# Kernel optimization log

Measured on AMD Instinct MI355X. Metric: run time of the kernel, lower is better.

The kernel has to match this reference:

```python
import jax, jax.numpy as jnp
import numpy as np

N = 200000   # real nodes
P = 10       # num_parts (virtual nodes)
IN = 256     # in_channels
HID = 256    # hidden_channels
DCD = 256    # decode_channels (use_jk=False -> == hidden)
OUT = 64     # out_channels


def layer_norm(x, g, b, eps=1e-5):
    mu = jnp.mean(x, axis=-1, keepdims=True)
    var = jnp.var(x, axis=-1, keepdims=True)
    return (x - mu) * jax.lax.rsqrt(var + eps) * g + b


def setup_inputs() -> dict:
    key = jax.random.key(0)
    ks = jax.random.split(key, 16)
    s = lambda d: 1.0 / np.sqrt(d)
    return {
        "x": jax.random.normal(ks[0], (N + P, IN), dtype=jnp.float32),
        "mapping": jax.random.randint(ks[1], (N,), 0, P, dtype=jnp.int32),
        "vnode_embed": jax.random.normal(ks[2], (P, IN), dtype=jnp.float32),
        "vnode_bias_hid": 0.1 * jax.random.normal(ks[3], (P, HID), dtype=jnp.float32),
        "vnode_bias_dcd": 0.1 * jax.random.normal(ks[4], (P, DCD), dtype=jnp.float32),
        "W_in2hid": s(IN) * jax.random.normal(ks[5], (IN, HID), dtype=jnp.float32),
        "b_in2hid": jnp.zeros((HID,), dtype=jnp.float32),
        "g_ln_hid": jnp.ones((HID,), dtype=jnp.float32),
        "b_ln_hid": jnp.zeros((HID,), dtype=jnp.float32),
        "W_enc": s(HID) * jax.random.normal(ks[6], (HID, DCD), dtype=jnp.float32),
        "b_enc": jnp.zeros((DCD,), dtype=jnp.float32),
        "g_ln_enc": jnp.ones((DCD,), dtype=jnp.float32),
        "b_ln_enc": jnp.zeros((DCD,), dtype=jnp.float32),
        "W_aggr": s(2 * DCD) * jax.random.normal(ks[7], (2 * DCD, DCD), dtype=jnp.float32),
        "b_aggr": jnp.zeros((DCD,), dtype=jnp.float32),
        "W_out": s(DCD) * jax.random.normal(ks[8], (DCD, OUT), dtype=jnp.float32),
        "b_out": jnp.zeros((OUT,), dtype=jnp.float32),
    }


def reference(x, mapping, vnode_embed, vnode_bias_hid, vnode_bias_dcd,
              W_in2hid, b_in2hid, g_ln_hid, b_ln_hid,
              W_enc, b_enc, g_ln_enc, b_ln_enc,
              W_aggr, b_aggr, W_out, b_out):
    p = vnode_embed.shape[0]
    n = x.shape[0] - p
    # overwrite virtual-node rows with learned embeddings
    x = x.at[-p:].set(vnode_embed)
    # in2hid -> LayerNorm -> ELU
    x = jax.nn.elu(layer_norm(x @ W_in2hid + b_in2hid, g_ln_hid, b_ln_hid))
    x = x.at[-p:].add(vnode_bias_hid)
    # encoder stub: single linear hidden->decode with ELU (loss := 0)
    x = jax.nn.elu(x @ W_enc + b_enc)
    # decode-stage virtual-node bias
    x = x.at[-p:].add(vnode_bias_dcd)
    v_x = x[-p:]                      # [P, DCD]
    gathered = v_x[mapping]           # irregular gather of virtual rows, [N, DCD]
    n_x = jnp.concatenate([x[:n], gathered], axis=1)   # [N, 2*DCD]
    n_x = jax.nn.elu(layer_norm(n_x @ W_aggr + b_aggr, g_ln_enc, b_ln_enc))
    # dropout: eval mode -> identity
    full = jnp.concatenate([n_x, v_x], axis=0)
    y = full @ W_out + b_out
    out = y[:n]                       # [N, OUT]
    return out
```

## Files before the change

### kernel.cpp

```cpp
#include <hip/hip_runtime.h>
#include <hip/hip_bf16.h>
#include <math.h>

typedef unsigned short u16;
typedef __attribute__((ext_vector_type(8))) short bf16x8;
typedef __attribute__((ext_vector_type(4))) float f32x4;
typedef __attribute__((ext_vector_type(4))) int i32x4;

#define PV 10

__device__ __forceinline__ float bf2f(u16 u){
  union{unsigned int i; float f;} v; v.i = ((unsigned int)u)<<16; return v.f;
}
__device__ __forceinline__ u16 f2bf(float f){
  union{float f; unsigned int i;} v; v.f = f;
  unsigned int r = (v.i + 0x7FFFu + ((v.i>>16)&1u))>>16;
  return (u16)r;
}
__device__ __forceinline__ float eluf(float z){
  return z > 0.f ? z : (__expf(z) - 1.f);
}
__device__ __forceinline__ float ldp(const void* p, int i, int f32f){
  return f32f ? ((const float*)p)[i] : bf2f(((const u16*)p)[i]);
}
__device__ __forceinline__ int swz(int row, int cb){
  int m = ((row & 7) << 4) ^ ((row & 8) << 2);
  return (row << 9) + (cb ^ m);
}

__global__ void k_sniff(const u16* __restrict__ x, int* __restrict__ flag){
  int t = threadIdx.x;
  u16 u = x[2*t];
  int e = (u >> 7) & 0xFF;
  int sane = (e >= 113 && e <= 134) ? 1 : 0;
  unsigned long long b = __ballot(sane);
  if (t == 0) *flag = (__popcll(b) < 32) ? 1 : 0;
}

__global__ void k_fragpack(const int* __restrict__ flagp,
                           const void* __restrict__ W1, const void* __restrict__ W2,
                           const void* __restrict__ Wa, const void* __restrict__ Wo,
                           u16* __restrict__ W1F, u16* __restrict__ W2F,
                           u16* __restrict__ WaF, u16* __restrict__ WoF)
{
  const int f = *flagp;
  int idx = blockIdx.x * 256 + threadIdx.x;
  if (idx < 196608) {
    int local = idx & 65535;
    int which = idx >> 16;
    int j = local & 7;
    int fid = local >> 3;
    int lane = fid & 63, q = lane & 15, g = lane >> 4;
    int n = (fid >> 6) & 3;
    int s = (fid >> 8) & 7;
    int w = (fid >> 11) & 3;
    int col = 64*w + 16*n + q;
    int k = 32*s + 8*g + j;
    const void* src = which == 0 ? W1 : (which == 1 ? W2 : Wa);
    u16* dst = which == 0 ? W1F : (which == 1 ? W2F : WaF);
    dst[local] = f2bf(ldp(src, k*256 + col, f));
  } else if (idx < 212992) {
    int local = idx - 196608;
    int j = local & 7;
    int fid = local >> 3;
    int lane = fid & 63, q = lane & 15, g = lane >> 4;
    int n = (fid >> 6) & 3;
    int s = (fid >> 8) & 7;
    int col = 16*n + q;
    int k = 32*s + 8*g + j;
    WoF[local] = f2bf(ldp(Wo, k*64 + col, f));
  }
}

__global__ void k_vnode(const int* __restrict__ flagp,
                        const void* __restrict__ embed, const void* __restrict__ W1,
                        const void* __restrict__ b1, const void* __restrict__ g1, const void* __restrict__ bb1,
                        const void* __restrict__ vbh,
                        const void* __restrict__ W2, const void* __restrict__ b2,
                        const void* __restrict__ vbd,
                        const void* __restrict__ Wa, const void* __restrict__ ba,
                        float* __restrict__ vg)
{
  __shared__ float buf[PV][256];
  __shared__ float st[PV][2];
  const int f = *flagp;
  const int t = threadIdx.x;
  const int lane = t & 63;
  const int w = t >> 6;

  for (int r=0;r<PV;r++) buf[r][t] = ldp(embed, r*256 + t, f);
  __syncthreads();

  float acc[PV];

  #pragma unroll
  for (int r=0;r<PV;r++) acc[r] = 0.f;
  for (int k8=0;k8<32;k8++){
    float wf[8];
    #pragma unroll
    for (int j=0;j<8;j++) wf[j] = ldp(W1, (k8*8+j)*256 + t, f);
    #pragma unroll
    for (int r=0;r<PV;r++){
      f32x4 a0 = *(const f32x4*)(&buf[r][k8*8]);
      f32x4 a1 = *(const f32x4*)(&buf[r][k8*8+4]);
      acc[r] = fmaf(a0[0],wf[0],acc[r]); acc[r] = fmaf(a0[1],wf[1],acc[r]);
      acc[r] = fmaf(a0[2],wf[2],acc[r]); acc[r] = fmaf(a0[3],wf[3],acc[r]);
      acc[r] = fmaf(a1[0],wf[4],acc[r]); acc[r] = fmaf(a1[1],wf[5],acc[r]);
      acc[r] = fmaf(a1[2],wf[6],acc[r]); acc[r] = fmaf(a1[3],wf[7],acc[r]);
    }
  }
  {
    float bv = ldp(b1, t, f);
    #pragma unroll
    for (int r=0;r<PV;r++) acc[r] += bv;
  }
  __syncthreads();
  #pragma unroll
  for (int r=0;r<PV;r++) buf[r][t] = acc[r];
  __syncthreads();
  for (int r = w; r < PV; r += 4){
    float v0=buf[r][lane], v1=buf[r][lane+64], v2=buf[r][lane+128], v3=buf[r][lane+192];
    float s = v0+v1+v2+v3;
    float ss = v0*v0+v1*v1+v2*v2+v3*v3;
    #pragma unroll
    for (int off=1; off<64; off<<=1){ s += __shfl_xor(s,off,64); ss += __shfl_xor(ss,off,64); }
    if (lane==0){
      float mu = s*(1.f/256.f);
      float var = ss*(1.f/256.f) - mu*mu;
      st[r][0]=mu; st[r][1]=rsqrtf(var+1e-5f);
    }
  }
  __syncthreads();
  {
    float gv = ldp(g1,t,f), bbv = ldp(bb1,t,f);
    #pragma unroll
    for (int r=0;r<PV;r++){
      float v = (acc[r]-st[r][0])*st[r][1]*gv + bbv;
      buf[r][t] = eluf(v) + ldp(vbh, r*256+t, f);
    }
  }
  __syncthreads();

  #pragma unroll
  for (int r=0;r<PV;r++) acc[r] = 0.f;
  for (int k8=0;k8<32;k8++){
    float wf[8];
    #pragma unroll
    for (int j=0;j<8;j++) wf[j] = ldp(W2, (k8*8+j)*256 + t, f);
    #pragma unroll
    for (int r=0;r<PV;r++){
      f32x4 a0 = *(const f32x4*)(&buf[r][k8*8]);
      f32x4 a1 = *(const f32x4*)(&buf[r][k8*8+4]);
      acc[r] = fmaf(a0[0],wf[0],acc[r]); acc[r] = fmaf(a0[1],wf[1],acc[r]);
      acc[r] = fmaf(a0[2],wf[2],acc[r]); acc[r] = fmaf(a0[3],wf[3],acc[r]);
      acc[r] = fmaf(a1[0],wf[4],acc[r]); acc[r] = fmaf(a1[1],wf[5],acc[r]);
      acc[r] = fmaf(a1[2],wf[6],acc[r]); acc[r] = fmaf(a1[3],wf[7],acc[r]);
    }
  }
  __syncthreads();
  {
    float bv = ldp(b2,t,f);
    #pragma unroll
    for (int r=0;r<PV;r++) buf[r][t] = eluf(acc[r]+bv) + ldp(vbd, r*256+t, f);
  }
  __syncthreads();

  #pragma unroll
  for (int r=0;r<PV;r++) acc[r] = 0.f;
  for (int k8=0;k8<32;k8++){
    float wf[8];
    #pragma unroll
    for (int j=0;j<8;j++) wf[j] = ldp(Wa, (256 + k8*8+j)*256 + t, f);
    #pragma unroll
    for (int r=0;r<PV;r++){
      f32x4 a0 = *(const f32x4*)(&buf[r][k8*8]);
      f32x4 a1 = *(const f32x4*)(&buf[r][k8*8+4]);
      acc[r] = fmaf(a0[0],wf[0],acc[r]); acc[r] = fmaf(a0[1],wf[1],acc[r]);
      acc[r] = fmaf(a0[2],wf[2],acc[r]); acc[r] = fmaf(a0[3],wf[3],acc[r]);
      acc[r] = fmaf(a1[0],wf[4],acc[r]); acc[r] = fmaf(a1[1],wf[5],acc[r]);
      acc[r] = fmaf(a1[2],wf[6],acc[r]); acc[r] = fmaf(a1[3],wf[7],acc[r]);
    }
  }
  {
    float bv = ldp(ba,t,f);
    #pragma unroll
    for (int r=0;r<PV;r++) vg[r*256+t] = acc[r] + bv;
  }
}

__device__ __forceinline__ void ln_rows(f32x4 (&acc)[4][4], float2 (*part)[4], float2* stats,
                                        int tid, int wid, int q, int g)
{
  #pragma unroll
  for (int m=0;m<4;m++){
    #pragma unroll
    for (int j=0;j<4;j++){
      float s1=0.f, s2=0.f;
      #pragma unroll
      for (int n=0;n<4;n++){ float v = acc[m][n][j]; s1+=v; s2+=v*v; }
      s1 += __shfl_xor(s1,1,64); s2 += __shfl_xor(s2,1,64);
      s1 += __shfl_xor(s1,2,64); s2 += __shfl_xor(s2,2,64);
      s1 += __shfl_xor(s1,4,64); s2 += __shfl_xor(s2,4,64);
      s1 += __shfl_xor(s1,8,64); s2 += __shfl_xor(s2,8,64);
      if (q == 0) part[16*m + 4*g + j][wid] = make_float2(s1, s2);
    }
  }
  __syncthreads();
  if (tid < 64){
    float s=0.f, ss=0.f;
    #pragma unroll
    for (int w=0;w<4;w++){ float2 p = part[tid][w]; s+=p.x; ss+=p.y; }
    float mu = s*(1.f/256.f);
    float var = ss*(1.f/256.f) - mu*mu;
    stats[tid] = make_float2(mu, rsqrtf(var + 1e-5f));
  }
  __syncthreads();
}

__global__ __launch_bounds__(256, 2) void k_main(
    const int* __restrict__ flagp,
    const void* __restrict__ x, const int* __restrict__ mapping,
    const void* __restrict__ b1, const void* __restrict__ g1, const void* __restrict__ bb1,
    const void* __restrict__ b2,
    const void* __restrict__ g3, const void* __restrict__ bb3,
    const void* __restrict__ bo,
    const u16* __restrict__ W1F, const u16* __restrict__ W2F,
    const u16* __restrict__ WaF, const u16* __restrict__ WoF,
    const float* __restrict__ vg, void* __restrict__ out)
{
  __shared__ __align__(16) u16 Abuf[64*256];
  __shared__ float2 part[64][4];
  __shared__ float2 stats[64];
  __shared__ int maplds[64];

  const int f = *flagp;
  const int tid = threadIdx.x;
  const int wid = tid >> 6;
  const int lane = tid & 63;
  const int q = lane & 15;
  const int g = lane >> 4;
  const int R0 = blockIdx.x * 64;

  if (f) {
    const float* xr = (const float*)x + (size_t)R0 * 256;
    #pragma unroll
    for (int i=0;i<8;i++){
      int c = tid + 256*i;
      int row = c >> 5;
      int cb  = (c & 31) << 4;
      int e0  = (c & 31) << 3;
      float4 a = *(const float4*)(xr + row*256 + e0);
      float4 b = *(const float4*)(xr + row*256 + e0 + 4);
      union { u16 h[8]; i32x4 v; } pk;
      pk.h[0]=f2bf(a.x); pk.h[1]=f2bf(a.y); pk.h[2]=f2bf(a.z); pk.h[3]=f2bf(a.w);
      pk.h[4]=f2bf(b.x); pk.h[5]=f2bf(b.y); pk.h[6]=f2bf(b.z); pk.h[7]=f2bf(b.w);
      *(i32x4*)((char*)Abuf + swz(row, cb)) = pk.v;
    }
  } else {
    const u16* xr = (const u16*)x + (size_t)R0 * 256;
    #pragma unroll
    for (int i=0;i<8;i++){
      int c = tid + 256*i;
      int row = c >> 5;
      int cb  = (c & 31) << 4;
      i32x4 v = *(const i32x4*)(xr + row*256 + ((c&31)<<3));
      *(i32x4*)((char*)Abuf + swz(row, cb)) = v;
    }
  }
  if (tid < 64){
    int mv = mapping[R0 + tid];
    maplds[tid] = mv < 0 ? 0 : (mv > PV-1 ? PV-1 : mv);
  }
  __syncthreads();

  f32x4 acc[4][4];
  const int fbase = wid*16384 + lane*8;

  {
    #pragma unroll
    for (int n=0;n<4;n++){
      float bv = ldp(b1, 64*wid + 16*n + q, f);
      #pragma unroll
      for (int m=0;m<4;m++) acc[m][n] = (f32x4){bv,bv,bv,bv};
    }
    #pragma unroll
    for (int s=0;s<8;s++){
      bf16x8 af[4], bw[4];
      #pragma unroll
      for (int m=0;m<4;m++) af[m] = *(const bf16x8*)((const char*)Abuf + swz(16*m+q, 64*s+16*g));
      #pragma unroll
      for (int n=0;n<4;n++) bw[n] = *(const bf16x8*)(W1F + fbase + (s*4+n)*512);
      #pragma unroll
      for (int m=0;m<4;m++){
        #pragma unroll
        for (int n=0;n<4;n++)
          acc[m][n] = __builtin_amdgcn_mfma_f32_16x16x32_bf16(af[m], bw[n], acc[m][n], 0,0,0);
      }
    }
  }
  ln_rows(acc, part, stats, tid, wid, q, g);
  {
    float gam[4], bet[4];
    #pragma unroll
    for (int n=0;n<4;n++){ int col = 64*wid+16*n+q; gam[n]=ldp(g1,col,f); bet[n]=ldp(bb1,col,f); }
    #pragma unroll
    for (int m=0;m<4;m++){
      #pragma unroll
      for (int j=0;j<4;j++){
        int row = 16*m + 4*g + j;
        float2 st = stats[row];
        #pragma unroll
        for (int n=0;n<4;n++){
          float v = (acc[m][n][j] - st.x) * st.y * gam[n] + bet[n];
          *(u16*)((char*)Abuf + swz(row, (64*wid+16*n+q)<<1)) = f2bf(eluf(v));
        }
      }
    }
  }
  __syncthreads();

  {
    #pragma unroll
    for (int n=0;n<4;n++){
      float bv = ldp(b2, 64*wid + 16*n + q, f);
      #pragma unroll
      for (int m=0;m<4;m++) acc[m][n] = (f32x4){bv,bv,bv,bv};
    }
    #pragma unroll
    for (int s=0;s<8;s++){
      bf16x8 af[4], bw[4];
      #pragma unroll
      for (int m=0;m<4;m++) af[m] = *(const bf16x8*)((const char*)Abuf + swz(16*m+q, 64*s+16*g));
      #pragma unroll
      for (int n=0;n<4;n++) bw[n] = *(const bf16x8*)(W2F + fbase + (s*4+n)*512);
      #pragma unroll
      for (int m=0;m<4;m++){
        #pragma unroll
        for (int n=0;n<4;n++)
          acc[m][n] = __builtin_amdgcn_mfma_f32_16x16x32_bf16(af[m], bw[n], acc[m][n], 0,0,0);
      }
    }
  }
  __syncthreads();
  {
    #pragma unroll
    for (int m=0;m<4;m++){
      #pragma unroll
      for (int j=0;j<4;j++){
        int row = 16*m + 4*g + j;
        #pragma unroll
        for (int n=0;n<4;n++)
          *(u16*)((char*)Abuf + swz(row, (64*wid+16*n+q)<<1)) = f2bf(eluf(acc[m][n][j]));
      }
    }
  }
  __syncthreads();

  {
    #pragma unroll
    for (int m=0;m<4;m++){
      int mp[4];
      #pragma unroll
      for (int j=0;j<4;j++) mp[j] = maplds[16*m + 4*g + j];
      #pragma unroll
      for (int n=0;n<4;n++){
        int col = 64*wid + 16*n + q;
        #pragma unroll
        for (int j=0;j<4;j++) acc[m][n][j] = vg[mp[j]*256 + col];
      }
    }
    #pragma unroll
    for (int s=0;s<8;s++){
      bf16x8 af[4], bw[4];
      #pragma unroll
      for (int m=0;m<4;m++) af[m] = *(const bf16x8*)((const char*)Abuf + swz(16*m+q, 64*s+16*g));
      #pragma unroll
      for (int n=0;n<4;n++) bw[n] = *(const bf16x8*)(WaF + fbase + (s*4+n)*512);
      #pragma unroll
      for (int m=0;m<4;m++){
        #pragma unroll
        for (int n=0;n<4;n++)
          acc[m][n] = __builtin_amdgcn_mfma_f32_16x16x32_bf16(af[m], bw[n], acc[m][n], 0,0,0);
      }
    }
  }
  ln_rows(acc, part, stats, tid, wid, q, g);
  {
    float gam[4], bet[4];
    #pragma unroll
    for (int n=0;n<4;n++){ int col = 64*wid+16*n+q; gam[n]=ldp(g3,col,f); bet[n]=ldp(bb3,col,f); }
    #pragma unroll
    for (int m=0;m<4;m++){
      #pragma unroll
      for (int j=0;j<4;j++){
        int row = 16*m + 4*g + j;
        float2 st = stats[row];
        #pragma unroll
        for (int n=0;n<4;n++){
          float v = (acc[m][n][j] - st.x) * st.y * gam[n] + bet[n];
          *(u16*)((char*)Abuf + swz(row, (64*wid+16*n+q)<<1)) = f2bf(eluf(v));
        }
      }
    }
  }
  __syncthreads();

  {
    f32x4 a4[4];
    #pragma unroll
    for (int n=0;n<4;n++){ float bv = ldp(bo, 16*n+q, f); a4[n] = (f32x4){bv,bv,bv,bv}; }
    #pragma unroll
    for (int s=0;s<8;s++){
      bf16x8 af = *(const bf16x8*)((const char*)Abuf + swz(16*wid+q, 64*s+16*g));
      #pragma unroll
      for (int n=0;n<4;n++){
        bf16x8 bw = *(const bf16x8*)(WoF + (s*4+n)*512 + lane*8);
        a4[n] = __builtin_amdgcn_mfma_f32_16x16x32_bf16(af, bw, a4[n], 0,0,0);
      }
    }
    if (f){
      float* outf = (float*)out;
      #pragma unroll
      for (int n=0;n<4;n++){
        #pragma unroll
        for (int j=0;j<4;j++){
          int grow = R0 + 16*wid + 4*g + j;
          outf[(size_t)grow*64 + 16*n + q] = a4[n][j];
        }
      }
    } else {
      u16* outh = (u16*)out;
      #pragma unroll
      for (int n=0;n<4;n++){
        #pragma unroll
        for (int j=0;j<4;j++){
          int grow = R0 + 16*wid + 4*g + j;
          outh[(size_t)grow*64 + 16*n + q] = f2bf(a4[n][j]);
        }
      }
    }
  }
}

extern "C" void kernel_launch(void* const* d_in, const int* in_sizes, int n_in,
                              void* d_out, int out_size, void* d_ws, size_t ws_size,
                              hipStream_t stream)
{
  const void* x    = d_in[0];
  const int* mapping = (const int*)d_in[1];
  const void* embed= d_in[2];
  const void* vbh  = d_in[3];
  const void* vbd  = d_in[4];
  const void* W1   = d_in[5];
  const void* b1   = d_in[6];
  const void* g1   = d_in[7];
  const void* bb1  = d_in[8];
  const void* W2   = d_in[9];
  const void* b2   = d_in[10];
  const void* g3   = d_in[11];
  const void* bb3  = d_in[12];
  const void* Wa   = d_in[13];
  const void* ba   = d_in[14];
  const void* Wo   = d_in[15];
  const void* bo   = d_in[16];

  char* ws = (char*)d_ws;
  int* flagp = (int*)ws;
  u16* W1F = (u16*)(ws + 4096);
  u16* W2F = (u16*)(ws + 4096 + 131072);
  u16* WaF = (u16*)(ws + 4096 + 262144);
  u16* WoF = (u16*)(ws + 4096 + 393216);
  float* vg = (float*)(ws + 4096 + 425984);

  const int N = in_sizes[1];

  k_sniff<<<1, 64, 0, stream>>>((const u16*)x, flagp);
  k_fragpack<<<832, 256, 0, stream>>>(flagp, W1, W2, Wa, Wo, W1F, W2F, WaF, WoF);
  k_vnode<<<1, 256, 0, stream>>>(flagp, embed, W1, b1, g1, bb1, vbh, W2, b2, vbd, Wa, ba, vg);
  k_main<<<N/64, 256, 0, stream>>>(flagp, x, mapping, b1, g1, bb1, b2, g3, bb3, bo,
                                   W1F, W2F, WaF, WoF, vg, (void*)d_out);
}
```

Before: 309.1 us.

## Double rows per block to 128 and use packed bf16 conversion

```diff
diff --git a/kernel.cpp b/kernel.cpp
--- a/kernel.cpp
+++ b/kernel.cpp
@@ -3,6 +3,7 @@
 #include <math.h>
 
 typedef unsigned short u16;
+typedef unsigned int u32;
 typedef __attribute__((ext_vector_type(8))) short bf16x8;
 typedef __attribute__((ext_vector_type(4))) float f32x4;
 typedef __attribute__((ext_vector_type(4))) int i32x4;
@@ -16,6 +17,9 @@
   union{float f; unsigned int i;} v; v.f = f;
   unsigned int r = (v.i + 0x7FFFu + ((v.i>>16)&1u))>>16;
   return (u16)r;
+}
+__device__ __forceinline__ u32 cvtpk(float lo, float hi){
+  u32 r; asm("v_cvt_pk_bf16_f32 %0, %1, %2" : "=v"(r) : "v"(lo), "v"(hi)); return r;
 }
 __device__ __forceinline__ float eluf(float z){
   return z > 0.f ? z : (__expf(z) - 1.f);
@@ -188,37 +192,9 @@
   }
 }
 
-__device__ __forceinline__ void ln_rows(f32x4 (&acc)[4][4], float2 (*part)[4], float2* stats,
-                                        int tid, int wid, int q, int g)
-{
-  #pragma unroll
-  for (int m=0;m<4;m++){
-    #pragma unroll
-    for (int j=0;j<4;j++){
-      float s1=0.f, s2=0.f;
-      #pragma unroll
-      for (int n=0;n<4;n++){ float v = acc[m][n][j]; s1+=v; s2+=v*v; }
-      s1 += __shfl_xor(s1,1,64); s2 += __shfl_xor(s2,1,64);
-      s1 += __shfl_xor(s1,2,64); s2 += __shfl_xor(s2,2,64);
-      s1 += __shfl_xor(s1,4,64); s2 += __shfl_xor(s2,4,64);
-      s1 += __shfl_xor(s1,8,64); s2 += __shfl_xor(s2,8,64);
-      if (q == 0) part[16*m + 4*g + j][wid] = make_float2(s1, s2);
-    }
-  }
-  __syncthreads();
-  if (tid < 64){
-    float s=0.f, ss=0.f;
-    #pragma unroll
-    for (int w=0;w<4;w++){ float2 p = part[tid][w]; s+=p.x; ss+=p.y; }
-    float mu = s*(1.f/256.f);
-    float var = ss*(1.f/256.f) - mu*mu;
-    stats[tid] = make_float2(mu, rsqrtf(var + 1e-5f));
-  }
-  __syncthreads();
-}
-
+#define MROWS 128
 __global__ __launch_bounds__(256, 2) void k_main(
-    const int* __restrict__ flagp,
+    const int* __restrict__ flagp, int N,
     const void* __restrict__ x, const int* __restrict__ mapping,
     const void* __restrict__ b1, const void* __restrict__ g1, const void* __restrict__ bb1,
     const void* __restrict__ b2,
@@ -228,10 +204,11 @@
     const u16* __restrict__ WaF, const u16* __restrict__ WoF,
     const float* __restrict__ vg, void* __restrict__ out)
 {
-  __shared__ __align__(16) u16 Abuf[64*256];
-  __shared__ float2 part[64][4];
-  __shared__ float2 stats[64];
-  __shared__ int maplds[64];
+  extern __shared__ __align__(16) char smem[];
+  u16* Abuf = (u16*)smem;
+  float2 (*part)[4] = (float2(*)[4])(smem + 65536);
+  float2* stats = (float2*)(smem + 69632);
+  int* maplds = (int*)(smem + 70656);
 
   const int f = *flagp;
   const int tid = threadIdx.x;
@@ -239,41 +216,47 @@
   const int lane = tid & 63;
   const int q = lane & 15;
   const int g = lane >> 4;
-  const int R0 = blockIdx.x * 64;
+  const int R0 = blockIdx.x * MROWS;
 
   if (f) {
     const float* xr = (const float*)x + (size_t)R0 * 256;
     #pragma unroll
-    for (int i=0;i<8;i++){
+    for (int i=0;i<16;i++){
       int c = tid + 256*i;
       int row = c >> 5;
       int cb  = (c & 31) << 4;
       int e0  = (c & 31) << 3;
-      float4 a = *(const float4*)(xr + row*256 + e0);
-      float4 b = *(const float4*)(xr + row*256 + e0 + 4);
-      union { u16 h[8]; i32x4 v; } pk;
-      pk.h[0]=f2bf(a.x); pk.h[1]=f2bf(a.y); pk.h[2]=f2bf(a.z); pk.h[3]=f2bf(a.w);
-      pk.h[4]=f2bf(b.x); pk.h[5]=f2bf(b.y); pk.h[6]=f2bf(b.z); pk.h[7]=f2bf(b.w);
-      *(i32x4*)((char*)Abuf + swz(row, cb)) = pk.v;
+      i32x4 v;
+      if (R0 + row < N){
+        float4 a = *(const float4*)(xr + row*256 + e0);
+        float4 b = *(const float4*)(xr + row*256 + e0 + 4);
+        union { u32 u[4]; i32x4 v; } pk;
+        pk.u[0]=cvtpk(a.x,a.y); pk.u[1]=cvtpk(a.z,a.w);
+        pk.u[2]=cvtpk(b.x,b.y); pk.u[3]=cvtpk(b.z,b.w);
+        v = pk.v;
+      } else v = (i32x4){0,0,0,0};
+      *(i32x4*)((char*)Abuf + swz(row, cb)) = v;
     }
   } else {
     const u16* xr = (const u16*)x + (size_t)R0 * 256;
     #pragma unroll
-    for (int i=0;i<8;i++){
+    for (int i=0;i<16;i++){
       int c = tid + 256*i;
       int row = c >> 5;
       int cb  = (c & 31) << 4;
-      i32x4 v = *(const i32x4*)(xr + row*256 + ((c&31)<<3));
+      i32x4 v = (R0 + row < N) ? *(const i32x4*)(xr + row*256 + ((c&31)<<3))
+                               : (i32x4){0,0,0,0};
       *(i32x4*)((char*)Abuf + swz(row, cb)) = v;
     }
   }
-  if (tid < 64){
-    int mv = mapping[R0 + tid];
+  if (tid < MROWS){
+    int idx = R0 + tid;
+    int mv = mapping[idx < N ? idx : 0];
     maplds[tid] = mv < 0 ? 0 : (mv > PV-1 ? PV-1 : mv);
   }
   __syncthreads();
 
-  f32x4 acc[4][4];
+  f32x4 acc[8][4];
   const int fbase = wid*16384 + lane*8;
 
   {
@@ -281,39 +264,69 @@
     for (int n=0;n<4;n++){
       float bv = ldp(b1, 64*wid + 16*n + q, f);
       #pragma unroll
-      for (int m=0;m<4;m++) acc[m][n] = (f32x4){bv,bv,bv,bv};
+      for (int m=0;m<8;m++) acc[m][n] = (f32x4){bv,bv,bv,bv};
     }
     #pragma unroll
     for (int s=0;s<8;s++){
-      bf16x8 af[4], bw[4];
-      #pragma unroll
-      for (int m=0;m<4;m++) af[m] = *(const bf16x8*)((const char*)Abuf + swz(16*m+q, 64*s+16*g));
+      bf16x8 af[8], bw[4];
+      #pragma unroll
+      for (int m=0;m<8;m++) af[m] = *(const bf16x8*)((const char*)Abuf + swz(16*m+q, 64*s+16*g));
       #pragma unroll
       for (int n=0;n<4;n++) bw[n] = *(const bf16x8*)(W1F + fbase + (s*4+n)*512);
       #pragma unroll
-      for (int m=0;m<4;m++){
+      for (int m=0;m<8;m++){
         #pragma unroll
         for (int n=0;n<4;n++)
           acc[m][n] = __builtin_amdgcn_mfma_f32_16x16x32_bf16(af[m], bw[n], acc[m][n], 0,0,0);
       }
     }
   }
-  ln_rows(acc, part, stats, tid, wid, q, g);
+  {
+    #pragma unroll
+    for (int m=0;m<8;m++){
+      #pragma unroll
+      for (int j=0;j<4;j++){
+        float s1=0.f, s2=0.f;
+        #pragma unroll
+        for (int n=0;n<4;n++){ float v = acc[m][n][j]; s1+=v; s2+=v*v; }
+        s1 += __shfl_xor(s1,1,64); s2 += __shfl_xor(s2,1,64);
+        s1 += __shfl_xor(s1,2,64); s2 += __shfl_xor(s2,2,64);
+        s1 += __shfl_xor(s1,4,64); s2 += __shfl_xor(s2,4,64);
+        s1 += __shfl_xor(s1,8,64); s2 += __shfl_xor(s2,8,64);
+        if (q == 0) part[16*m + 4*g + j][wid] = make_float2(s1, s2);
+      }
+    }
+    __syncthreads();
+    if (tid < MROWS){
+      float s=0.f, ss=0.f;
+      #pragma unroll
+      for (int w=0;w<4;w++){ float2 p = part[tid][w]; s+=p.x; ss+=p.y; }
+      float mu = s*(1.f/256.f);
+      float var = ss*(1.f/256.f) - mu*mu;
+      stats[tid] = make_float2(mu, rsqrtf(var + 1e-5f));
+    }
+    __syncthreads();
+  }
   {
     float gam[4], bet[4];
     #pragma unroll
     for (int n=0;n<4;n++){ int col = 64*wid+16*n+q; gam[n]=ldp(g1,col,f); bet[n]=ldp(bb1,col,f); }
     #pragma unroll
-    for (int m=0;m<4;m++){
-      #pragma unroll
-      for (int j=0;j<4;j++){
-        int row = 16*m + 4*g + j;
-        float2 st = stats[row];
-        #pragma unroll
-        for (int n=0;n<4;n++){
-          float v = (acc[m][n][j] - st.x) * st.y * gam[n] + bet[n];
-          *(u16*)((char*)Abuf + swz(row, (64*wid+16*n+q)<<1)) = f2bf(eluf(v));
+    for (int m=0;m<8;m++){
+      float v[4];
+      #pragma unroll
+      for (int n=0;n<4;n++){
+        #pragma unroll
+        for (int j=0;j<4;j++){
+          float2 st = stats[16*m + 4*g + j];
+          v[j] = eluf((acc[m][n][j] - st.x) * st.y * gam[n] + bet[n]);
         }
+        u32 u01 = cvtpk(v[0],v[1]), u23 = cvtpk(v[2],v[3]);
+        int col2 = (64*wid+16*n+q)<<1;
+        *(u16*)((char*)Abuf + swz(16*m+4*g+0, col2)) = (u16)u01;
+        *(u16*)((char*)Abuf + swz(16*m+4*g+1, col2)) = (u16)(u01>>16);
+        *(u16*)((char*)Abuf + swz(16*m+4*g+2, col2)) = (u16)u23;
+        *(u16*)((char*)Abuf + swz(16*m+4*g+3, col2)) = (u16)(u23>>16);
       }
     }
   }
@@ -324,17 +337,17 @@
     for (int n=0;n<4;n++){
       float bv = ldp(b2, 64*wid + 16*n + q, f);
       #pragma unroll
-      for (int m=0;m<4;m++) acc[m][n] = (f32x4){bv,bv,bv,bv};
+      for (int m=0;m<8;m++) acc[m][n] = (f32x4){bv,bv,bv,bv};
     }
     #pragma unroll
     for (int s=0;s<8;s++){
-      bf16x8 af[4], bw[4];
-      #pragma unroll
-      for (int m=0;m<4;m++) af[m] = *(const bf16x8*)((const char*)Abuf + swz(16*m+q, 64*s+16*g));
+      bf16x8 af[8], bw[4];
+      #pragma unroll
+      for (int m=0;m<8;m++) af[m] = *(const bf16x8*)((const char*)Abuf + swz(16*m+q, 64*s+16*g));
       #pragma unroll
       for (int n=0;n<4;n++) bw[n] = *(const bf16x8*)(W2F + fbase + (s*4+n)*512);
       #pragma unroll
-      for (int m=0;m<4;m++){
+      for (int m=0;m<8;m++){
         #pragma unroll
         for (int n=0;n<4;n++)
           acc[m][n] = __builtin_amdgcn_mfma_f32_16x16x32_bf16(af[m], bw[n], acc[m][n], 0,0,0);
@@ -344,21 +357,26 @@
   __syncthreads();
   {
     #pragma unroll
-    for (int m=0;m<4;m++){
-      #pragma unroll
-      for (int j=0;j<4;j++){
-        int row = 16*m + 4*g + j;
-        #pragma unroll
-        for (int n=0;n<4;n++)
-          *(u16*)((char*)Abuf + swz(row, (64*wid+16*n+q)<<1)) = f2bf(eluf(acc[m][n][j]));
-      }
-    }
-  }
-  __syncthreads();
-
-  {
-    #pragma unroll
-    for (int m=0;m<4;m++){
+    for (int m=0;m<8;m++){
+      #pragma unroll
+      for (int n=0;n<4;n++){
+        float v[4];
+        #pragma unroll
+        for (int j=0;j<4;j++) v[j] = eluf(acc[m][n][j]);
+        u32 u01 = cvtpk(v[0],v[1]), u23 = cvtpk(v[2],v[3]);
+        int col2 = (64*wid+16*n+q)<<1;
+        *(u16*)((char*)Abuf + swz(16*m+4*g+0, col2)) = (u16)u01;
+        *(u16*)((char*)Abuf + swz(16*m+4*g+1, col2)) = (u16)(u01>>16);
+        *(u16*)((char*)Abuf + swz(16*m+4*g+2, col2)) = (u16)u23;
+        *(u16*)((char*)Abuf + swz(16*m+4*g+3, col2)) = (u16)(u23>>16);
+      }
+    }
+  }
+  __syncthreads();
+
+  {
+    #pragma unroll
+    for (int m=0;m<8;m++){
       int mp[4];
       #pragma unroll
       for (int j=0;j<4;j++) mp[j] = maplds[16*m + 4*g + j];
@@ -371,71 +389,100 @@
     }
     #pragma unroll
     for (int s=0;s<8;s++){
-      bf16x8 af[4], bw[4];
-      #pragma unroll
-      for (int m=0;m<4;m++) af[m] = *(const bf16x8*)((const char*)Abuf + swz(16*m+q, 64*s+16*g));
+      bf16x8 af[8], bw[4];
+      #pragma unroll
+      for (int m=0;m<8;m++) af[m] = *(const bf16x8*)((const char*)Abuf + swz(16*m+q, 64*s+16*g));
       #pragma unroll
       for (int n=0;n<4;n++) bw[n] = *(const bf16x8*)(WaF + fbase + (s*4+n)*512);
       #pragma unroll
-      for (int m=0;m<4;m++){
+      for (int m=0;m<8;m++){
         #pragma unroll
         for (int n=0;n<4;n++)
           acc[m][n] = __builtin_amdgcn_mfma_f32_16x16x32_bf16(af[m], bw[n], acc[m][n], 0,0,0);
       }
     }
   }
-  ln_rows(acc, part, stats, tid, wid, q, g);
+  {
+    #pragma unroll
+    for (int m=0;m<8;m++){
+      #pragma unroll
+      for (int j=0;j<4;j++){
+        float s1=0.f, s2=0.f;
+        #pragma unroll
+        for (int n=0;n<4;n++){ float v = acc[m][n][j]; s1+=v; s2+=v*v; }
+        s1 += __shfl_xor(s1,1,64); s2 += __shfl_xor(s2,1,64);
+        s1 += __shfl_xor(s1,2,64); s2 += __shfl_xor(s2,2,64);
+        s1 += __shfl_xor(s1,4,64); s2 += __shfl_xor(s2,4,64);
+        s1 += __shfl_xor(s1,8,64); s2 += __shfl_xor(s2,8,64);
+        if (q == 0) part[16*m + 4*g + j][wid] = make_float2(s1, s2);
+      }
+    }
+    __syncthreads();
+    if (tid < MROWS){
+      float s=0.f, ss=0.f;
+      #pragma unroll
+      for (int w=0;w<4;w++){ float2 p = part[tid][w]; s+=p.x; ss+=p.y; }
+      float mu = s*(1.f/256.f);
+      float var = ss*(1.f/256.f) - mu*mu;
+      stats[tid] = make_float2(mu, rsqrtf(var + 1e-5f));
+    }
+    __syncthreads();
+  }
   {
     float gam[4], bet[4];
     #pragma unroll
     for (int n=0;n<4;n++){ int col = 64*wid+16*n+q; gam[n]=ldp(g3,col,f); bet[n]=ldp(bb3,col,f); }
     #pragma unroll
-    for (int m=0;m<4;m++){
-      #pragma unroll
-      for (int j=0;j<4;j++){
-        int row = 16*m + 4*g + j;
-        float2 st = stats[row];
-        #pragma unroll
-        for (int n=0;n<4;n++){
-          float v = (acc[m][n][j] - st.x) * st.y * gam[n] + bet[n];
-          *(u16*)((char*)Abuf + swz(row, (64*wid+16*n+q)<<1)) = f2bf(eluf(v));
+    for (int m=0;m<8;m++){
+      #pragma unroll
+      for (int n=0;n<4;n++){
+        float v[4];
+        #pragma unroll
+        for (int j=0;j<4;j++){
+          float2 st = stats[16*m + 4*g + j];
+          v[j] = eluf((acc[m][n][j] - st.x) * st.y * gam[n] + bet[n]);
         }
-      }
-    }
-  }
-  __syncthreads();
-
-  {
-    f32x4 a4[4];
-    #pragma unroll
-    for (int n=0;n<4;n++){ float bv = ldp(bo, 16*n+q, f); a4[n] = (f32x4){bv,bv,bv,bv}; }
+        u32 u01 = cvtpk(v[0],v[1]), u23 = cvtpk(v[2],v[3]);
+        int col2 = (64*wid+16*n+q)<<1;
+        *(u16*)((char*)Abuf + swz(16*m+4*g+0, col2)) = (u16)u01;
+        *(u16*)((char*)Abuf + swz(16*m+4*g+1, col2)) = (u16)(u01>>16);
+        *(u16*)((char*)Abuf + swz(16*m+4*g+2, col2)) = (u16)u23;
+        *(u16*)((char*)Abuf + swz(16*m+4*g+3, col2)) = (u16)(u23>>16);
+      }
+    }
+  }
+  __syncthreads();
+
+  {
+    f32x4 a4[2][4];
+    #pragma unroll
+    for (int n=0;n<4;n++){
+      float bv = ldp(bo, 16*n+q, f);
+      a4[0][n] = (f32x4){bv,bv,bv,bv};
+      a4[1][n] = (f32x4){bv,bv,bv,bv};
+    }
     #pragma unroll
     for (int s=0;s<8;s++){
-      bf16x8 af = *(const bf16x8*)((const char*)Abuf + swz(16*wid+q, 64*s+16*g));
+      bf16x8 af0 = *(const bf16x8*)((const char*)Abuf + swz(32*wid+q, 64*s+16*g));
+      bf16x8 af1 = *(const bf16x8*)((const char*)Abuf + swz(32*wid+16+q, 64*s+16*g));
       #pragma unroll
       for (int n=0;n<4;n++){
         bf16x8 bw = *(const bf16x8*)(WoF + (s*4+n)*512 + lane*8);
-        a4[n] = __builtin_amdgcn_mfma_f32_16x16x32_bf16(af, bw, a4[n], 0,0,0);
-      }
-    }
-    if (f){
-      float* outf = (float*)out;
+        a4[0][n] = __builtin_amdgcn_mfma_f32_16x16x32_bf16(af0, bw, a4[0][n], 0,0,0);
+        a4[1][n] = __builtin_amdgcn_mfma_f32_16x16x32_bf16(af1, bw, a4[1][n], 0,0,0);
+      }
+    }
+    #pragma unroll
+    for (int mm=0;mm<2;mm++){
       #pragma unroll
       for (int n=0;n<4;n++){
         #pragma unroll
         for (int j=0;j<4;j++){
-          int grow = R0 + 16*wid + 4*g + j;
-          outf[(size_t)grow*64 + 16*n + q] = a4[n][j];
-        }
-      }
-    } else {
-      u16* outh = (u16*)out;
-      #pragma unroll
-      for (int n=0;n<4;n++){
-        #pragma unroll
-        for (int j=0;j<4;j++){
-          int grow = R0 + 16*wid + 4*g + j;
-          outh[(size_t)grow*64 + 16*n + q] = f2bf(a4[n][j]);
+          int grow = R0 + 32*wid + 16*mm + 4*g + j;
+          if (grow < N){
+            if (f) ((float*)out)[(size_t)grow*64 + 16*n + q] = a4[mm][n][j];
+            else   ((u16*)out)[(size_t)grow*64 + 16*n + q] = f2bf(a4[mm][n][j]);
+          }
         }
       }
     }
@@ -474,9 +521,16 @@
 
   const int N = in_sizes[1];
 
+  static int attr_set = 0;
+  if (!attr_set){
+    hipFuncSetAttribute((const void*)k_main, hipFuncAttributeMaxDynamicSharedMemorySize, 71168);
+    attr_set = 1;
+  }
+
   k_sniff<<<1, 64, 0, stream>>>((const u16*)x, flagp);
   k_fragpack<<<832, 256, 0, stream>>>(flagp, W1, W2, Wa, Wo, W1F, W2F, WaF, WoF);
   k_vnode<<<1, 256, 0, stream>>>(flagp, embed, W1, b1, g1, bb1, vbh, W2, b2, vbd, Wa, ba, vg);
-  k_main<<<N/64, 256, 0, stream>>>(flagp, x, mapping, b1, g1, bb1, b2, g3, bb3, bo,
-                                   W1F, W2F, WaF, WoF, vg, (void*)d_out);
-}
+  int grid = (N + MROWS - 1) / MROWS;
+  k_main<<<grid, 256, 71168, stream>>>(flagp, N, x, mapping, b1, g1, bb1, b2, g3, bb3, bo,
+                                       W1F, W2F, WaF, WoF, vg, (void*)d_out);
+}
```

Measured after the change: 494.5 us. +60.0%, slower.

## Load x straight into MFMA fragments, use packed bf16 converts, stage output stores

Applied to the files above, without the earlier changes.

```diff
diff --git a/kernel.cpp b/kernel.cpp
--- a/kernel.cpp
+++ b/kernel.cpp
@@ -3,6 +3,7 @@
 #include <math.h>
 
 typedef unsigned short u16;
+typedef unsigned int u32;
 typedef __attribute__((ext_vector_type(8))) short bf16x8;
 typedef __attribute__((ext_vector_type(4))) float f32x4;
 typedef __attribute__((ext_vector_type(4))) int i32x4;
@@ -16,6 +17,9 @@
   union{float f; unsigned int i;} v; v.f = f;
   unsigned int r = (v.i + 0x7FFFu + ((v.i>>16)&1u))>>16;
   return (u16)r;
+}
+__device__ __forceinline__ u32 cvtpk(float lo, float hi){
+  u32 r; asm("v_cvt_pk_bf16_f32 %0, %1, %2" : "=v"(r) : "v"(lo), "v"(hi)); return r;
 }
 __device__ __forceinline__ float eluf(float z){
   return z > 0.f ? z : (__expf(z) - 1.f);
@@ -217,7 +221,7 @@
   __syncthreads();
 }
 
-__global__ __launch_bounds__(256, 2) void k_main(
+__global__ __launch_bounds__(256, 3) void k_main(
     const int* __restrict__ flagp,
     const void* __restrict__ x, const int* __restrict__ mapping,
     const void* __restrict__ b1, const void* __restrict__ g1, const void* __restrict__ bb1,
@@ -241,37 +245,10 @@
   const int g = lane >> 4;
   const int R0 = blockIdx.x * 64;
 
-  if (f) {
-    const float* xr = (const float*)x + (size_t)R0 * 256;
-    #pragma unroll
-    for (int i=0;i<8;i++){
-      int c = tid + 256*i;
-      int row = c >> 5;
-      int cb  = (c & 31) << 4;
-      int e0  = (c & 31) << 3;
-      float4 a = *(const float4*)(xr + row*256 + e0);
-      float4 b = *(const float4*)(xr + row*256 + e0 + 4);
-      union { u16 h[8]; i32x4 v; } pk;
-      pk.h[0]=f2bf(a.x); pk.h[1]=f2bf(a.y); pk.h[2]=f2bf(a.z); pk.h[3]=f2bf(a.w);
-      pk.h[4]=f2bf(b.x); pk.h[5]=f2bf(b.y); pk.h[6]=f2bf(b.z); pk.h[7]=f2bf(b.w);
-      *(i32x4*)((char*)Abuf + swz(row, cb)) = pk.v;
-    }
-  } else {
-    const u16* xr = (const u16*)x + (size_t)R0 * 256;
-    #pragma unroll
-    for (int i=0;i<8;i++){
-      int c = tid + 256*i;
-      int row = c >> 5;
-      int cb  = (c & 31) << 4;
-      i32x4 v = *(const i32x4*)(xr + row*256 + ((c&31)<<3));
-      *(i32x4*)((char*)Abuf + swz(row, cb)) = v;
-    }
-  }
   if (tid < 64){
     int mv = mapping[R0 + tid];
     maplds[tid] = mv < 0 ? 0 : (mv > PV-1 ? PV-1 : mv);
   }
-  __syncthreads();
 
   f32x4 acc[4][4];
   const int fbase = wid*16384 + lane*8;
@@ -283,13 +260,88 @@
       #pragma unroll
       for (int m=0;m<4;m++) acc[m][n] = (f32x4){bv,bv,bv,bv};
     }
+    if (f){
+      const float* xb = (const float*)x + (size_t)R0 * 256;
+      #pragma unroll
+      for (int s=0;s<8;s++){
+        bf16x8 af[4], bw[4];
+        #pragma unroll
+        for (int m=0;m<4;m++){
+          const float* p = xb + (16*m+q)*256 + 32*s + 8*g;
+          float4 a = *(const float4*)p;
+          float4 b = *(const float4*)(p+4);
+          union{ u32 u[4]; bf16x8 v8; } pk;
+          pk.u[0]=cvtpk(a.x,a.y); pk.u[1]=cvtpk(a.z,a.w);
+          pk.u[2]=cvtpk(b.x,b.y); pk.u[3]=cvtpk(b.z,b.w);
+          af[m] = pk.v8;
+        }
+        #pragma unroll
+        for (int n=0;n<4;n++) bw[n] = *(const bf16x8*)(W1F + fbase + (s*4+n)*512);
+        #pragma unroll
+        for (int m=0;m<4;m++){
+          #pragma unroll
+          for (int n=0;n<4;n++)
+            acc[m][n] = __builtin_amdgcn_mfma_f32_16x16x32_bf16(af[m], bw[n], acc[m][n], 0,0,0);
+        }
+      }
+    } else {
+      const u16* xb = (const u16*)x + (size_t)R0 * 256;
+      #pragma unroll
+      for (int s=0;s<8;s++){
+        bf16x8 af[4], bw[4];
+        #pragma unroll
+        for (int m=0;m<4;m++) af[m] = *(const bf16x8*)(xb + (16*m+q)*256 + 32*s + 8*g);
+        #pragma unroll
+        for (int n=0;n<4;n++) bw[n] = *(const bf16x8*)(W1F + fbase + (s*4+n)*512);
+        #pragma unroll
+        for (int m=0;m<4;m++){
+          #pragma unroll
+          for (int n=0;n<4;n++)
+            acc[m][n] = __builtin_amdgcn_mfma_f32_16x16x32_bf16(af[m], bw[n], acc[m][n], 0,0,0);
+        }
+      }
+    }
+  }
+  ln_rows(acc, part, stats, tid, wid, q, g);
+  {
+    float gam[4], bet[4];
+    #pragma unroll
+    for (int n=0;n<4;n++){ int col = 64*wid+16*n+q; gam[n]=ldp(g1,col,f); bet[n]=ldp(bb1,col,f); }
+    #pragma unroll
+    for (int m=0;m<4;m++){
+      #pragma unroll
+      for (int n=0;n<4;n++){
+        float v[4];
+        #pragma unroll
+        for (int j=0;j<4;j++){
+          float2 st = stats[16*m + 4*g + j];
+          v[j] = eluf((acc[m][n][j] - st.x) * st.y * gam[n] + bet[n]);
+        }
+        u32 u01 = cvtpk(v[0],v[1]), u23 = cvtpk(v[2],v[3]);
+        int col2 = (64*wid+16*n+q)<<1;
+        *(u16*)((char*)Abuf + swz(16*m+4*g+0, col2)) = (u16)u01;
+        *(u16*)((char*)Abuf + swz(16*m+4*g+1, col2)) = (u16)(u01>>16);
+        *(u16*)((char*)Abuf + swz(16*m+4*g+2, col2)) = (u16)u23;
+        *(u16*)((char*)Abuf + swz(16*m+4*g+3, col2)) = (u16)(u23>>16);
+      }
+    }
+  }
+  __syncthreads();
+
+  {
+    #pragma unroll
+    for (int n=0;n<4;n++){
+      float bv = ldp(b2, 64*wid + 16*n + q, f);
+      #pragma unroll
+      for (int m=0;m<4;m++) acc[m][n] = (f32x4){bv,bv,bv,bv};
+    }
     #pragma unroll
     for (int s=0;s<8;s++){
       bf16x8 af[4], bw[4];
       #pragma unroll
       for (int m=0;m<4;m++) af[m] = *(const bf16x8*)((const char*)Abuf + swz(16*m+q, 64*s+16*g));
       #pragma unroll
-      for (int n=0;n<4;n++) bw[n] = *(const bf16x8*)(W1F + fbase + (s*4+n)*512);
+      for (int n=0;n<4;n++) bw[n] = *(const bf16x8*)(W2F + fbase + (s*4+n)*512);
       #pragma unroll
       for (int m=0;m<4;m++){
         #pragma unroll
@@ -298,33 +350,38 @@
       }
     }
   }
-  ln_rows(acc, part, stats, tid, wid, q, g);
-  {
-    float gam[4], bet[4];
-    #pragma unroll
-    for (int n=0;n<4;n++){ int col = 64*wid+16*n+q; gam[n]=ldp(g1,col,f); bet[n]=ldp(bb1,col,f); }
+  __syncthreads();
+  {
     #pragma unroll
     for (int m=0;m<4;m++){
       #pragma unroll
-      for (int j=0;j<4;j++){
-        int row = 16*m + 4*g + j;
-        float2 st = stats[row];
-        #pragma unroll
-        for (int n=0;n<4;n++){
-          float v = (acc[m][n][j] - st.x) * st.y * gam[n] + bet[n];
-          *(u16*)((char*)Abuf + swz(row, (64*wid+16*n+q)<<1)) = f2bf(eluf(v));
-        }
-      }
-    }
-  }
-  __syncthreads();
-
-  {
-    #pragma unroll
-    for (int n=0;n<4;n++){
-      float bv = ldp(b2, 64*wid + 16*n + q, f);
-      #pragma unroll
-      for (int m=0;m<4;m++) acc[m][n] = (f32x4){bv,bv,bv,bv};
+      for (int n=0;n<4;n++){
+        float v[4];
+        #pragma unroll
+        for (int j=0;j<4;j++) v[j] = eluf(acc[m][n][j]);
+        u32 u01 = cvtpk(v[0],v[1]), u23 = cvtpk(v[2],v[3]);
+        int col2 = (64*wid+16*n+q)<<1;
+        *(u16*)((char*)Abuf + swz(16*m+4*g+0, col2)) = (u16)u01;
+        *(u16*)((char*)Abuf + swz(16*m+4*g+1, col2)) = (u16)(u01>>16);
+        *(u16*)((char*)Abuf + swz(16*m+4*g+2, col2)) = (u16)u23;
+        *(u16*)((char*)Abuf + swz(16*m+4*g+3, col2)) = (u16)(u23>>16);
+      }
+    }
+  }
+  __syncthreads();
+
+  {
+    #pragma unroll
+    for (int m=0;m<4;m++){
+      int mp[4];
+      #pragma unroll
+      for (int j=0;j<4;j++) mp[j] = maplds[16*m + 4*g + j];
+      #pragma unroll
+      for (int n=0;n<4;n++){
+        int col = 64*wid + 16*n + q;
+        #pragma unroll
+        for (int j=0;j<4;j++) acc[m][n][j] = vg[mp[j]*256 + col];
+      }
     }
     #pragma unroll
     for (int s=0;s<8;s++){
@@ -332,7 +389,7 @@
       #pragma unroll
       for (int m=0;m<4;m++) af[m] = *(const bf16x8*)((const char*)Abuf + swz(16*m+q, 64*s+16*g));
       #pragma unroll
-      for (int n=0;n<4;n++) bw[n] = *(const bf16x8*)(W2F + fbase + (s*4+n)*512);
+      for (int n=0;n<4;n++) bw[n] = *(const bf16x8*)(WaF + fbase + (s*4+n)*512);
       #pragma unroll
       for (int m=0;m<4;m++){
         #pragma unroll
@@ -341,65 +398,27 @@
       }
     }
   }
-  __syncthreads();
-  {
+  ln_rows(acc, part, stats, tid, wid, q, g);
+  {
+    float gam[4], bet[4];
+    #pragma unroll
+    for (int n=0;n<4;n++){ int col = 64*wid+16*n+q; gam[n]=ldp(g3,col,f); bet[n]=ldp(bb3,col,f); }
     #pragma unroll
     for (int m=0;m<4;m++){
       #pragma unroll
-      for (int j=0;j<4;j++){
-        int row = 16*m + 4*g + j;
-        #pragma unroll
-        for (int n=0;n<4;n++)
-          *(u16*)((char*)Abuf + swz(row, (64*wid+16*n+q)<<1)) = f2bf(eluf(acc[m][n][j]));
-      }
-    }
-  }
-  __syncthreads();
-
-  {
-    #pragma unroll
-    for (int m=0;m<4;m++){
-      int mp[4];
-      #pragma unroll
-      for (int j=0;j<4;j++) mp[j] = maplds[16*m + 4*g + j];
-      #pragma unroll
-      for (int n=0;n<4;n++){
-        int col = 64*wid + 16*n + q;
-        #pragma unroll
-        for (int j=0;j<4;j++) acc[m][n][j] = vg[mp[j]*256 + col];
-      }
-    }
-    #pragma unroll
-    for (int s=0;s<8;s++){
-      bf16x8 af[4], bw[4];
-      #pragma unroll
-      for (int m=0;m<4;m++) af[m] = *(const bf16x8*)((const char*)Abuf + swz(16*m+q, 64*s+16*g));
-      #pragma unroll
-      for (int n=0;n<4;n++) bw[n] = *(const bf16x8*)(WaF + fbase + (s*4+n)*512);
-      #pragma unroll
-      for (int m=0;m<4;m++){
-        #pragma unroll
-        for (int n=0;n<4;n++)
-          acc[m][n] = __builtin_amdgcn_mfma_f32_16x16x32_bf16(af[m], bw[n], acc[m][n], 0,0,0);
-      }
-    }
-  }
-  ln_rows(acc, part, stats, tid, wid, q, g);
-  {
-    float gam[4], bet[4];
-    #pragma unroll
-    for (int n=0;n<4;n++){ int col = 64*wid+16*n+q; gam[n]=ldp(g3,col,f); bet[n]=ldp(bb3,col,f); }
-    #pragma unroll
-    for (int m=0;m<4;m++){
-      #pragma unroll
-      for (int j=0;j<4;j++){
-        int row = 16*m + 4*g + j;
-        float2 st = stats[row];
-        #pragma unroll
-        for (int n=0;n<4;n++){
-          float v = (acc[m][n][j] - st.x) * st.y * gam[n] + bet[n];
-          *(u16*)((char*)Abuf + swz(row, (64*wid+16*n+q)<<1)) = f2bf(eluf(v));
+      for (int n=0;n<4;n++){
+        float v[4];
+        #pragma unroll
+        for (int j=0;j<4;j++){
+          float2 st = stats[16*m + 4*g + j];
+          v[j] = eluf((acc[m][n][j] - st.x) * st.y * gam[n] + bet[n]);
         }
+        u32 u01 = cvtpk(v[0],v[1]), u23 = cvtpk(v[2],v[3]);
+        int col2 = (64*wid+16*n+q)<<1;
+        *(u16*)((char*)Abuf + swz(16*m+4*g+0, col2)) = (u16)u01;
+        *(u16*)((char*)Abuf + swz(16*m+4*g+1, col2)) = (u16)(u01>>16);
+        *(u16*)((char*)Abuf + swz(16*m+4*g+2, col2)) = (u16)u23;
+        *(u16*)((char*)Abuf + swz(16*m+4*g+3, col2)) = (u16)(u23>>16);
       }
     }
   }
@@ -419,15 +438,26 @@
       }
     }
     if (f){
-      float* outf = (float*)out;
-      #pragma unroll
-      for (int n=0;n<4;n++){
-        #pragma unroll
-        for (int j=0;j<4;j++){
-          int grow = R0 + 16*wid + 4*g + j;
-          outf[(size_t)grow*64 + 16*n + q] = a4[n][j];
-        }
-      }
+      __syncthreads();
+      float* obuf = (float*)Abuf;
+      #pragma unroll
+      for (int n=0;n<4;n++){
+        #pragma unroll
+        for (int j=0;j<4;j++)
+          obuf[(16*wid + 4*g + j)*68 + 16*n + q] = a4[n][j];
+      }
+      __syncthreads();
+      int row = tid >> 2, c0 = (tid & 3) * 16;
+      const float* src = obuf + row*68 + c0;
+      float* dst = (float*)out + (size_t)(R0 + row)*64 + c0;
+      f32x4 v0 = *(const f32x4*)(src);
+      f32x4 v1 = *(const f32x4*)(src + 4);
+      f32x4 v2 = *(const f32x4*)(src + 8);
+      f32x4 v3 = *(const f32x4*)(src + 12);
+      *(f32x4*)(dst)      = v0;
+      *(f32x4*)(dst + 4)  = v1;
+      *(f32x4*)(dst + 8)  = v2;
+      *(f32x4*)(dst + 12) = v3;
     } else {
       u16* outh = (u16*)out;
       #pragma unroll
```

New measurement: 442.7 us. 43.2% more time.
